# Kernel optimization log

Measured on AMD Instinct MI355X. Metric: run time of the kernel, lower is better.

## Reference

```python
import jax, jax.numpy as jnp
import numpy as np

V, E, DIN, DH = 8192, 4096, 512, 256
N_CLASSES = 2
EPS = 1e-5  # torch LayerNorm default
EDGE_P = 0.004  # ~33 nodes per hyperedge


def layernorm(x, g, b):
    m = jnp.mean(x, axis=-1, keepdims=True)
    v = jnp.mean((x - m) ** 2, axis=-1, keepdims=True)
    return (x - m) / jnp.sqrt(v + EPS) * g + b


def setup_inputs() -> dict:
    key = jax.random.key(0)
    ks = jax.random.split(key, 8)
    X = jax.random.normal(ks[0], (V, DIN), dtype=jnp.float32)
    # binary incidence matrix (|V|, |E|)
    H_inc = (jax.random.uniform(ks[1], (V, E)) < EDGE_P).astype(jnp.float32)
    Wp = jax.random.normal(ks[2], (DH, DIN), dtype=jnp.float32) * 0.02  # input_proj (no bias)
    W0 = jax.random.normal(ks[3], (DH, DH), dtype=jnp.float32) * 0.02
    W1 = jax.random.normal(ks[4], (DH, DH), dtype=jnp.float32) * 0.02
    g0 = jnp.ones((DH,), jnp.float32); b0 = jnp.zeros((DH,), jnp.float32)
    g1 = jnp.ones((DH,), jnp.float32); b1 = jnp.zeros((DH,), jnp.float32)
    Wc = jax.random.normal(ks[5], (N_CLASSES, DH), dtype=jnp.float32) * 0.02
    bc = jnp.zeros((N_CLASSES,), jnp.float32)
    return {"X": X, "H_inc": H_inc, "Wp": Wp, "W0": W0, "W1": W1,
            "g0": g0, "b0": b0, "g1": g1, "b1": b1, "Wc": Wc, "bc": bc}


def reference(X, H_inc, Wp, W0, W1, g0, b0, g1, b1, Wc, bc):
    # --- normalized incidence: H_tilde = D_v^{-1/2} H D_e^{-1/2}, 0 for isolated ---
    d_v = H_inc.sum(axis=1)   # (V,)
    d_e = H_inc.sum(axis=0)   # (E,)
    dvi = jnp.where(d_v > 0, jnp.where(d_v > 0, d_v, 1.0) ** -0.5, 0.0)
    dei = jnp.where(d_e > 0, jnp.where(d_e > 0, d_e, 1.0) ** -0.5, 0.0)
    H_tilde = dvi[:, None] * H_inc * dei[None, :]            # (V, E)
    HHt = H_tilde @ H_tilde.T                                # (V, V)

    # input projection
    Xh = X @ Wp.T                                            # (V, DH)

    # L=2 message-passing layers with residual + LayerNorm
    for W, g, b in ((W0, g0, b0), (W1, g1, b1)):
        Xn = jax.nn.relu((HHt @ Xh) @ W.T)
        Xh = layernorm(Xh + Xn, g, b)

    # mean pool per hyperedge (== Python loop over E in the original):
    # z_e = mean of member node embeddings; zeros for empty hyperedges
    cnt = jnp.where(d_e > 0, d_e, 1.0)[:, None]              # (E, 1)
    z_E = (H_inc.T @ Xh) / cnt                               # (E, DH)

    logits = z_E @ Wc.T + bc                                 # (E, 2)
    return jax.nn.softmax(logits, axis=1)
```

## Files before the change

kernel.cpp:

```cpp
#include <hip/hip_runtime.h>
#include <math.h>

#define NV 8192
#define NE 4096
#define DIN 512
#define DH 256
#define CAP_E 96
#define CAP_V 64

#define OFF_XH   0
#define OFF_Z    (OFF_XH + NV*DH)
#define OFF_Y    (OFF_Z  + NV*DH)
#define OFF_NCNT (OFF_Y  + NE*DH)
#define OFF_ECNT (OFF_NCNT + NV)
#define OFF_EL   (OFF_ECNT + NE)
#define OFF_NL   (OFF_EL + NE*CAP_E)

using bf16x8 = __attribute__((ext_vector_type(8))) short;
using f32x4  = __attribute__((ext_vector_type(4))) float;

__device__ inline unsigned short f2bf(float f) {
    union { float f; unsigned u; } v; v.f = f;
    unsigned r = v.u + 0x7FFF + ((v.u >> 16) & 1);
    return (unsigned short)(r >> 16);
}

__global__ __launch_bounds__(256) void scan_H(const float* __restrict__ H,
                                              int* __restrict__ edge_cnt,
                                              int* __restrict__ node_cnt,
                                              int* __restrict__ edge_list,
                                              int* __restrict__ node_list) {
    int idx = blockIdx.x * 256 + threadIdx.x;
    int f0 = idx * 16;
    int v = f0 >> 12;
    int e = f0 & (NE - 1);
    float4 h0 = *(const float4*)(H + (size_t)f0);
    float4 h1 = *(const float4*)(H + (size_t)f0 + 4);
    float4 h2 = *(const float4*)(H + (size_t)f0 + 8);
    float4 h3 = *(const float4*)(H + (size_t)f0 + 12);
    float hv[16] = {h0.x, h0.y, h0.z, h0.w, h1.x, h1.y, h1.z, h1.w,
                    h2.x, h2.y, h2.z, h2.w, h3.x, h3.y, h3.z, h3.w};
    bool any = false;
#pragma unroll
    for (int j = 0; j < 16; ++j) any |= (hv[j] != 0.0f);
    if (__ballot(any) == 0ull) return;
#pragma unroll
    for (int j = 0; j < 16; ++j) {
        if (hv[j] != 0.0f) {
            int ee = e + j;
            int s1 = atomicAdd(&edge_cnt[ee], 1);
            if (s1 < CAP_E) edge_list[ee * CAP_E + s1] = v;
            int s2 = atomicAdd(&node_cnt[v], 1);
            if (s2 < CAP_V) node_list[v * CAP_V + s2] = ee;
        }
    }
}

__global__ __launch_bounds__(256) void gemm_bf16(const float* __restrict__ A,
                                                 const float* __restrict__ B,
                                                 float* __restrict__ C,
                                                 int K) {
    __shared__ short As[2048];
    __shared__ short Bs[16384];
    const int tid  = threadIdx.x;
    const int lane = tid & 63;
    const int w    = tid >> 6;
    const int bm   = blockIdx.x * 32;
    const int swz  = lane ^ ((lane >> 3) & 6);

    float4 ar[2], br[16];
    {
        int i0 = tid, i1 = tid + 256;
        ar[0] = *(const float4*)(A + (size_t)(bm + (i0 >> 4)) * K + ((i0 & 15) << 2));
        ar[1] = *(const float4*)(A + (size_t)(bm + (i1 >> 4)) * K + ((i1 & 15) << 2));
#pragma unroll
        for (int it = 0; it < 16; ++it) {
            int i = tid + it * 256;
            br[it] = *(const float4*)(B + (size_t)(i >> 4) * K + ((i & 15) << 2));
        }
    }
    f32x4 acc[2][4];
#pragma unroll
    for (int mi = 0; mi < 2; ++mi)
#pragma unroll
        for (int ni = 0; ni < 4; ++ni) acc[mi][ni] = (f32x4){0.f, 0.f, 0.f, 0.f};

    for (int k0 = 0; k0 < K; k0 += 64) {
        __syncthreads();
#pragma unroll
        for (int s = 0; s < 2; ++s) {
            int i = tid + s * 256;
            int row = i >> 4, kk = (i & 15) << 2;
            int kc = kk >> 5, quad = (kk >> 3) & 3, j = kk & 7;
            int ln = (row & 15) + (quad << 4);
            int p  = ln ^ ((ln >> 3) & 6);
            int addr = ((row >> 4) * 2 + kc) * 512 + p * 8 + j;
            float4 v = ar[s];
            ushort4 u = {f2bf(v.x), f2bf(v.y), f2bf(v.z), f2bf(v.w)};
            *(ushort4*)&As[addr] = u;
        }
#pragma unroll
        for (int it = 0; it < 16; ++it) {
            int i = tid + it * 256;
            int row = i >> 4, kk = (i & 15) << 2;
            int kc = kk >> 5, quad = (kk >> 3) & 3, j = kk & 7;
            int ln = (row & 15) + (quad << 4);
            int p  = ln ^ ((ln >> 3) & 6);
            int addr = ((row >> 4) * 2 + kc) * 512 + p * 8 + j;
            float4 v = br[it];
            ushort4 u = {f2bf(v.x), f2bf(v.y), f2bf(v.z), f2bf(v.w)};
            *(ushort4*)&Bs[addr] = u;
        }
        __syncthreads();
        if (k0 + 64 < K) {
            int kn = k0 + 64;
            int i0 = tid, i1 = tid + 256;
            ar[0] = *(const float4*)(A + (size_t)(bm + (i0 >> 4)) * K + kn + ((i0 & 15) << 2));
            ar[1] = *(const float4*)(A + (size_t)(bm + (i1 >> 4)) * K + kn + ((i1 & 15) << 2));
#pragma unroll
            for (int it = 0; it < 16; ++it) {
                int i = tid + it * 256;
                br[it] = *(const float4*)(B + (size_t)(i >> 4) * K + kn + ((i & 15) << 2));
            }
        }
#pragma unroll
        for (int kc = 0; kc < 2; ++kc) {
            bf16x8 af[2], bfr[4];
            af[0] = *(const bf16x8*)&As[(0 * 2 + kc) * 512 + swz * 8];
            af[1] = *(const bf16x8*)&As[(1 * 2 + kc) * 512 + swz * 8];
#pragma unroll
            for (int ni = 0; ni < 4; ++ni)
                bfr[ni] = *(const bf16x8*)&Bs[((w * 4 + ni) * 2 + kc) * 512 + swz * 8];
#pragma unroll
            for (int mi = 0; mi < 2; ++mi)
#pragma unroll
                for (int ni = 0; ni < 4; ++ni)
                    acc[mi][ni] = __builtin_amdgcn_mfma_f32_16x16x32_bf16(
                        af[mi], bfr[ni], acc[mi][ni], 0, 0, 0);
        }
    }
    const int quad = lane >> 4, cl = lane & 15;
#pragma unroll
    for (int mi = 0; mi < 2; ++mi)
#pragma unroll
        for (int ni = 0; ni < 4; ++ni)
#pragma unroll
            for (int r = 0; r < 4; ++r)
                C[(size_t)(bm + mi * 16 + quad * 4 + r) * DH + w * 64 + ni * 16 + cl]
                    = acc[mi][ni][r];
}

__global__ __launch_bounds__(256) void gemm_relu_res_ln(const float* __restrict__ Z,
                                                        const float* __restrict__ W,
                                                        float* __restrict__ Xh,
                                                        const float* __restrict__ g,
                                                        const float* __restrict__ b) {
    const int K = DH;
    __shared__ short As[2048];
    __shared__ short Bs[16384];
    __shared__ float redS[32][4];
    __shared__ float redQ[32][4];
    const int tid  = threadIdx.x;
    const int lane = tid & 63;
    const int w    = tid >> 6;
    const int bm   = blockIdx.x * 32;
    const int swz  = lane ^ ((lane >> 3) & 6);

    float4 ar[2], br[16];
    {
        int i0 = tid, i1 = tid + 256;
        ar[0] = *(const float4*)(Z + (size_t)(bm + (i0 >> 4)) * K + ((i0 & 15) << 2));
        ar[1] = *(const float4*)(Z + (size_t)(bm + (i1 >> 4)) * K + ((i1 & 15) << 2));
#pragma unroll
        for (int it = 0; it < 16; ++it) {
            int i = tid + it * 256;
            br[it] = *(const float4*)(W + (size_t)(i >> 4) * K + ((i & 15) << 2));
        }
    }
    f32x4 acc[2][4];
#pragma unroll
    for (int mi = 0; mi < 2; ++mi)
#pragma unroll
        for (int ni = 0; ni < 4; ++ni) acc[mi][ni] = (f32x4){0.f, 0.f, 0.f, 0.f};

    for (int k0 = 0; k0 < K; k0 += 64) {
        __syncthreads();
#pragma unroll
        for (int s = 0; s < 2; ++s) {
            int i = tid + s * 256;
            int row = i >> 4, kk = (i & 15) << 2;
            int kc = kk >> 5, quad = (kk >> 3) & 3, j = kk & 7;
            int ln = (row & 15) + (quad << 4);
            int p  = ln ^ ((ln >> 3) & 6);
            int addr = ((row >> 4) * 2 + kc) * 512 + p * 8 + j;
            float4 v = ar[s];
            ushort4 u = {f2bf(v.x), f2bf(v.y), f2bf(v.z), f2bf(v.w)};
            *(ushort4*)&As[addr] = u;
        }
#pragma unroll
        for (int it = 0; it < 16; ++it) {
            int i = tid + it * 256;
            int row = i >> 4, kk = (i & 15) << 2;
            int kc = kk >> 5, quad = (kk >> 3) & 3, j = kk & 7;
            int ln = (row & 15) + (quad << 4);
            int p  = ln ^ ((ln >> 3) & 6);
            int addr = ((row >> 4) * 2 + kc) * 512 + p * 8 + j;
            float4 v = br[it];
            ushort4 u = {f2bf(v.x), f2bf(v.y), f2bf(v.z), f2bf(v.w)};
            *(ushort4*)&Bs[addr] = u;
        }
        __syncthreads();
        if (k0 + 64 < K) {
            int kn = k0 + 64;
            int i0 = tid, i1 = tid + 256;
            ar[0] = *(const float4*)(Z + (size_t)(bm + (i0 >> 4)) * K + kn + ((i0 & 15) << 2));
            ar[1] = *(const float4*)(Z + (size_t)(bm + (i1 >> 4)) * K + kn + ((i1 & 15) << 2));
#pragma unroll
            for (int it = 0; it < 16; ++it) {
                int i = tid + it * 256;
                br[it] = *(const float4*)(W + (size_t)(i >> 4) * K + kn + ((i & 15) << 2));
            }
        }
#pragma unroll
        for (int kc = 0; kc < 2; ++kc) {
            bf16x8 af[2], bfr[4];
            af[0] = *(const bf16x8*)&As[(0 * 2 + kc) * 512 + swz * 8];
            af[1] = *(const bf16x8*)&As[(1 * 2 + kc) * 512 + swz * 8];
#pragma unroll
            for (int ni = 0; ni < 4; ++ni)
                bfr[ni] = *(const bf16x8*)&Bs[((w * 4 + ni) * 2 + kc) * 512 + swz * 8];
#pragma unroll
            for (int mi = 0; mi < 2; ++mi)
#pragma unroll
                for (int ni = 0; ni < 4; ++ni)
                    acc[mi][ni] = __builtin_amdgcn_mfma_f32_16x16x32_bf16(
                        af[mi], bfr[ni], acc[mi][ni], 0, 0, 0);
        }
    }
    const int quad = lane >> 4, cl = lane & 15;
#pragma unroll
    for (int mi = 0; mi < 2; ++mi)
#pragma unroll
        for (int r = 0; r < 4; ++r) {
            int row = bm + mi * 16 + quad * 4 + r;
            float s = 0.f, q = 0.f;
#pragma unroll
            for (int ni = 0; ni < 4; ++ni) {
                int col = w * 64 + ni * 16 + cl;
                float v = fmaxf(acc[mi][ni][r], 0.f) + Xh[(size_t)row * DH + col];
                acc[mi][ni][r] = v;
                s += v; q = fmaf(v, v, q);
            }
#pragma unroll
            for (int o = 1; o < 16; o <<= 1) {
                s += __shfl_xor(s, o, 64);
                q += __shfl_xor(q, o, 64);
            }
            if (cl == 0) {
                redS[mi * 16 + quad * 4 + r][w] = s;
                redQ[mi * 16 + quad * 4 + r][w] = q;
            }
        }
    __syncthreads();
#pragma unroll
    for (int mi = 0; mi < 2; ++mi)
#pragma unroll
        for (int r = 0; r < 4; ++r) {
            int R = mi * 16 + quad * 4 + r;
            float s = redS[R][0] + redS[R][1] + redS[R][2] + redS[R][3];
            float q = redQ[R][0] + redQ[R][1] + redQ[R][2] + redQ[R][3];
            float m = s * (1.0f / DH);
            float var = q * (1.0f / DH) - m * m;
            float rstd = rsqrtf(var + 1e-5f);
            int row = bm + R;
#pragma unroll
            for (int ni = 0; ni < 4; ++ni) {
                int col = w * 64 + ni * 16 + cl;
                float v = (acc[mi][ni][r] - m) * rstd * g[col] + b[col];
                Xh[(size_t)row * DH + col] = v;
            }
        }
}

__global__ __launch_bounds__(64) void edge_gather(const float* __restrict__ Xh,
                                                  const int* __restrict__ edge_cnt,
                                                  const int* __restrict__ edge_list,
                                                  const int* __restrict__ node_cnt,
                                                  float* __restrict__ Y) {
    int e = blockIdx.x;
    int tid = threadIdx.x;
    __shared__ int   lv[CAP_E];
    __shared__ float lc[CAP_E];
    int cnt = min(edge_cnt[e], CAP_E);
    for (int j = tid; j < cnt; j += 64) {
        int v = edge_list[e * CAP_E + j];
        lv[j] = v * (DH / 4);
        lc[j] = rsqrtf((float)node_cnt[v]);
    }
    __syncthreads();
    const float4* X4 = (const float4*)Xh;
    float4 a0 = {0,0,0,0}, a1 = {0,0,0,0}, a2 = {0,0,0,0}, a3 = {0,0,0,0};
    int i = 0;
    for (; i + 4 <= cnt; i += 4) {
        float4 x0 = X4[lv[i+0] + tid], x1 = X4[lv[i+1] + tid];
        float4 x2 = X4[lv[i+2] + tid], x3 = X4[lv[i+3] + tid];
        float c0 = lc[i+0], c1 = lc[i+1], c2 = lc[i+2], c3 = lc[i+3];
        a0.x = fmaf(c0, x0.x, a0.x); a0.y = fmaf(c0, x0.y, a0.y);
        a0.z = fmaf(c0, x0.z, a0.z); a0.w = fmaf(c0, x0.w, a0.w);
        a1.x = fmaf(c1, x1.x, a1.x); a1.y = fmaf(c1, x1.y, a1.y);
        a1.z = fmaf(c1, x1.z, a1.z); a1.w = fmaf(c1, x1.w, a1.w);
        a2.x = fmaf(c2, x2.x, a2.x); a2.y = fmaf(c2, x2.y, a2.y);
        a2.z = fmaf(c2, x2.z, a2.z); a2.w = fmaf(c2, x2.w, a2.w);
        a3.x = fmaf(c3, x3.x, a3.x); a3.y = fmaf(c3, x3.y, a3.y);
        a3.z = fmaf(c3, x3.z, a3.z); a3.w = fmaf(c3, x3.w, a3.w);
    }
    for (; i < cnt; ++i) {
        float4 x0 = X4[lv[i] + tid]; float c0 = lc[i];
        a0.x = fmaf(c0, x0.x, a0.x); a0.y = fmaf(c0, x0.y, a0.y);
        a0.z = fmaf(c0, x0.z, a0.z); a0.w = fmaf(c0, x0.w, a0.w);
    }
    float de = cnt > 0 ? rsqrtf((float)cnt) : 0.f;
    float4 o;
    o.x = de * ((a0.x + a1.x) + (a2.x + a3.x));
    o.y = de * ((a0.y + a1.y) + (a2.y + a3.y));
    o.z = de * ((a0.z + a1.z) + (a2.z + a3.z));
    o.w = de * ((a0.w + a1.w) + (a2.w + a3.w));
    ((float4*)Y)[e * (DH / 4) + tid] = o;
}

__global__ __launch_bounds__(64) void node_gather(const float* __restrict__ Y,
                                                  const int* __restrict__ node_cnt,
                                                  const int* __restrict__ node_list,
                                                  const int* __restrict__ edge_cnt,
                                                  float* __restrict__ Z) {
    int v = blockIdx.x;
    int tid = threadIdx.x;
    __shared__ int   le[CAP_V];
    __shared__ float lc[CAP_V];
    int cnt = min(node_cnt[v], CAP_V);
    if (tid < cnt) {
        int e = node_list[v * CAP_V + tid];
        le[tid] = e * (DH / 4);
        lc[tid] = rsqrtf((float)edge_cnt[e]);
    }
    __syncthreads();
    const float4* Y4 = (const float4*)Y;
    float4 a0 = {0,0,0,0}, a1 = {0,0,0,0}, a2 = {0,0,0,0}, a3 = {0,0,0,0};
    int i = 0;
    for (; i + 4 <= cnt; i += 4) {
        float4 x0 = Y4[le[i+0] + tid], x1 = Y4[le[i+1] + tid];
        float4 x2 = Y4[le[i+2] + tid], x3 = Y4[le[i+3] + tid];
        float c0 = lc[i+0], c1 = lc[i+1], c2 = lc[i+2], c3 = lc[i+3];
        a0.x = fmaf(c0, x0.x, a0.x); a0.y = fmaf(c0, x0.y, a0.y);
        a0.z = fmaf(c0, x0.z, a0.z); a0.w = fmaf(c0, x0.w, a0.w);
        a1.x = fmaf(c1, x1.x, a1.x); a1.y = fmaf(c1, x1.y, a1.y);
        a1.z = fmaf(c1, x1.z, a1.z); a1.w = fmaf(c1, x1.w, a1.w);
        a2.x = fmaf(c2, x2.x, a2.x); a2.y = fmaf(c2, x2.y, a2.y);
        a2.z = fmaf(c2, x2.z, a2.z); a2.w = fmaf(c2, x2.w, a2.w);
        a3.x = fmaf(c3, x3.x, a3.x); a3.y = fmaf(c3, x3.y, a3.y);
        a3.z = fmaf(c3, x3.z, a3.z); a3.w = fmaf(c3, x3.w, a3.w);
    }
    for (; i < cnt; ++i) {
        float4 x0 = Y4[le[i] + tid]; float c0 = lc[i];
        a0.x = fmaf(c0, x0.x, a0.x); a0.y = fmaf(c0, x0.y, a0.y);
        a0.z = fmaf(c0, x0.z, a0.z); a0.w = fmaf(c0, x0.w, a0.w);
    }
    float dv = cnt > 0 ? rsqrtf((float)cnt) : 0.f;
    float4 o;
    o.x = dv * ((a0.x + a1.x) + (a2.x + a3.x));
    o.y = dv * ((a0.y + a1.y) + (a2.y + a3.y));
    o.z = dv * ((a0.z + a1.z) + (a2.z + a3.z));
    o.w = dv * ((a0.w + a1.w) + (a2.w + a3.w));
    ((float4*)Z)[v * (DH / 4) + tid] = o;
}

__global__ __launch_bounds__(64) void pool_classify(const float* __restrict__ Xh,
                                                    const int* __restrict__ edge_cnt,
                                                    const int* __restrict__ edge_list,
                                                    const float* __restrict__ Wc,
                                                    const float* __restrict__ bc,
                                                    float* __restrict__ out) {
    int e = blockIdx.x;
    int tid = threadIdx.x;
    __shared__ int lv[CAP_E];
    int cnt = min(edge_cnt[e], CAP_E);
    for (int j = tid; j < cnt; j += 64) lv[j] = edge_list[e * CAP_E + j] * (DH / 4);
    __syncthreads();
    const float4* X4 = (const float4*)Xh;
    float4 a0 = {0,0,0,0}, a1 = {0,0,0,0}, a2 = {0,0,0,0}, a3 = {0,0,0,0};
    int i = 0;
    for (; i + 4 <= cnt; i += 4) {
        float4 x0 = X4[lv[i+0] + tid], x1 = X4[lv[i+1] + tid];
        float4 x2 = X4[lv[i+2] + tid], x3 = X4[lv[i+3] + tid];
        a0.x += x0.x; a0.y += x0.y; a0.z += x0.z; a0.w += x0.w;
        a1.x += x1.x; a1.y += x1.y; a1.z += x1.z; a1.w += x1.w;
        a2.x += x2.x; a2.y += x2.y; a2.z += x2.z; a2.w += x2.w;
        a3.x += x3.x; a3.y += x3.y; a3.z += x3.z; a3.w += x3.w;
    }
    for (; i < cnt; ++i) {
        float4 x0 = X4[lv[i] + tid];
        a0.x += x0.x; a0.y += x0.y; a0.z += x0.z; a0.w += x0.w;
    }
    float inv = cnt > 0 ? 1.0f / (float)cnt : 1.0f;
    float4 val;
    val.x = inv * ((a0.x + a1.x) + (a2.x + a3.x));
    val.y = inv * ((a0.y + a1.y) + (a2.y + a3.y));
    val.z = inv * ((a0.z + a1.z) + (a2.z + a3.z));
    val.w = inv * ((a0.w + a1.w) + (a2.w + a3.w));
    const float4* W4 = (const float4*)Wc;
    float4 w0 = W4[tid], w1 = W4[64 + tid];
    float p0 = val.x * w0.x + val.y * w0.y + val.z * w0.z + val.w * w0.w;
    float p1 = val.x * w1.x + val.y * w1.y + val.z * w1.z + val.w * w1.w;
#pragma unroll
    for (int o = 32; o > 0; o >>= 1) {
        p0 += __shfl_down(p0, o, 64);
        p1 += __shfl_down(p1, o, 64);
    }
    if (tid == 0) {
        float l0 = p0 + bc[0], l1 = p1 + bc[1];
        float mx = fmaxf(l0, l1);
        float e0 = expf(l0 - mx), e1 = expf(l1 - mx);
        float s = 1.0f / (e0 + e1);
        out[e * 2 + 0] = e0 * s;
        out[e * 2 + 1] = e1 * s;
    }
}

extern "C" void kernel_launch(void* const* d_in, const int* in_sizes, int n_in,
                              void* d_out, int out_size, void* d_ws, size_t ws_size,
                              hipStream_t stream) {
    const float* X  = (const float*)d_in[0];
    const float* H  = (const float*)d_in[1];
    const float* Wp = (const float*)d_in[2];
    const float* W0 = (const float*)d_in[3];
    const float* W1 = (const float*)d_in[4];
    const float* g0 = (const float*)d_in[5];
    const float* b0 = (const float*)d_in[6];
    const float* g1 = (const float*)d_in[7];
    const float* b1 = (const float*)d_in[8];
    const float* Wc = (const float*)d_in[9];
    const float* bc = (const float*)d_in[10];
    float* out = (float*)d_out;

    float* ws = (float*)d_ws;
    float* Xh  = ws + OFF_XH;
    float* Z   = ws + OFF_Z;
    float* Y   = ws + OFF_Y;
    int* node_cnt  = (int*)(ws + OFF_NCNT);
    int* edge_cnt  = (int*)(ws + OFF_ECNT);
    int* edge_list = (int*)(ws + OFF_EL);
    int* node_list = (int*)(ws + OFF_NL);

    hipMemsetAsync(node_cnt, 0, (size_t)(NV + NE) * sizeof(int), stream);

    scan_H<<<(NV * NE) / 4096, 256, 0, stream>>>(H, edge_cnt, node_cnt, edge_list, node_list);

    gemm_bf16<<<NV / 32, 256, 0, stream>>>(X, Wp, Xh, DIN);

    const float* Ws[2] = {W0, W1};
    const float* gs[2] = {g0, g1};
    const float* bs[2] = {b0, b1};
    for (int l = 0; l < 2; ++l) {
        edge_gather<<<NE, 64, 0, stream>>>(Xh, edge_cnt, edge_list, node_cnt, Y);
        node_gather<<<NV, 64, 0, stream>>>(Y, node_cnt, node_list, edge_cnt, Z);
        gemm_relu_res_ln<<<NV / 32, 256, 0, stream>>>(Z, Ws[l], Xh, gs[l], bs[l]);
    }

    pool_classify<<<NE, 64, 0, stream>>>(Xh, edge_cnt, edge_list, Wc, bc, out);
}
```

Baseline: 329.7 us.

## Build node lists in shared memory, pad edge counters, unroll gathers by eight

The incidence scan now uses one block per node row. Each node's edge list is collected in shared memory with a local atomic and written out once, which removes the global atomics on node counters. Edge counters are padded to one per 64 bytes to reduce atomic contention and false sharing between neighbouring hyperedges. The gather kernels use eight independent accumulators instead of four, putting more loads in flight. This adds more registers and a larger memset.

```diff
diff --git a/kernel.cpp b/kernel.cpp
--- a/kernel.cpp
+++ b/kernel.cpp
@@ -13,7 +13,7 @@
 #define OFF_Y    (OFF_Z  + NV*DH)
 #define OFF_NCNT (OFF_Y  + NE*DH)
 #define OFF_ECNT (OFF_NCNT + NV)
-#define OFF_EL   (OFF_ECNT + NE)
+#define OFF_EL   (OFF_ECNT + NE*16)
 #define OFF_NL   (OFF_EL + NE*CAP_E)
 
 using bf16x8 = __attribute__((ext_vector_type(8))) short;
@@ -30,30 +30,36 @@
                                               int* __restrict__ node_cnt,
                                               int* __restrict__ edge_list,
                                               int* __restrict__ node_list) {
-    int idx = blockIdx.x * 256 + threadIdx.x;
-    int f0 = idx * 16;
-    int v = f0 >> 12;
-    int e = f0 & (NE - 1);
-    float4 h0 = *(const float4*)(H + (size_t)f0);
-    float4 h1 = *(const float4*)(H + (size_t)f0 + 4);
-    float4 h2 = *(const float4*)(H + (size_t)f0 + 8);
-    float4 h3 = *(const float4*)(H + (size_t)f0 + 12);
+    int v = blockIdx.x;
+    int t = threadIdx.x;
+    __shared__ int lcnt;
+    __shared__ int lbuf[CAP_V];
+    if (t == 0) lcnt = 0;
+    __syncthreads();
+    const float4* H4 = (const float4*)(H + (size_t)v * NE);
+    float4 h0 = H4[t * 4 + 0], h1 = H4[t * 4 + 1];
+    float4 h2 = H4[t * 4 + 2], h3 = H4[t * 4 + 3];
     float hv[16] = {h0.x, h0.y, h0.z, h0.w, h1.x, h1.y, h1.z, h1.w,
                     h2.x, h2.y, h2.z, h2.w, h3.x, h3.y, h3.z, h3.w};
-    bool any = false;
-#pragma unroll
-    for (int j = 0; j < 16; ++j) any |= (hv[j] != 0.0f);
-    if (__ballot(any) == 0ull) return;
-#pragma unroll
-    for (int j = 0; j < 16; ++j) {
-        if (hv[j] != 0.0f) {
-            int ee = e + j;
-            int s1 = atomicAdd(&edge_cnt[ee], 1);
-            if (s1 < CAP_E) edge_list[ee * CAP_E + s1] = v;
-            int s2 = atomicAdd(&node_cnt[v], 1);
-            if (s2 < CAP_V) node_list[v * CAP_V + s2] = ee;
-        }
-    }
+    int myE[16]; int n = 0;
+    int e0 = t * 16;
+#pragma unroll
+    for (int j = 0; j < 16; ++j)
+        if (hv[j] != 0.0f) myE[n++] = e0 + j;
+    if (n > 0) {
+        int s = atomicAdd(&lcnt, n);
+        for (int k = 0; k < n; ++k) {
+            int ee = myE[k];
+            if (s + k < CAP_V) lbuf[s + k] = ee;
+            int g = atomicAdd(&edge_cnt[ee << 4], 1);
+            if (g < CAP_E) edge_list[ee * CAP_E + g] = v;
+        }
+    }
+    __syncthreads();
+    int c = lcnt;
+    if (t == 0) node_cnt[v] = c;
+    c = min(c, CAP_V);
+    for (int i = t; i < c; i += 256) node_list[v * CAP_V + i] = lbuf[i];
 }
 
 __global__ __launch_bounds__(256) void gemm_bf16(const float* __restrict__ A,
@@ -282,6 +288,28 @@
         }
 }
 
+#define GATHER_BODY(SRC, IDX, COEF, CNT)                                         \
+    float4 a[8];                                                                 \
+    _Pragma("unroll") for (int u = 0; u < 8; ++u) a[u] = (float4){0,0,0,0};      \
+    int i = 0;                                                                   \
+    for (; i + 8 <= CNT; i += 8) {                                               \
+        _Pragma("unroll") for (int u = 0; u < 8; ++u) {                          \
+            float4 x = SRC[IDX[i+u] + tid]; float c = COEF[i+u];                 \
+            a[u].x = fmaf(c, x.x, a[u].x); a[u].y = fmaf(c, x.y, a[u].y);        \
+            a[u].z = fmaf(c, x.z, a[u].z); a[u].w = fmaf(c, x.w, a[u].w);        \
+        }                                                                        \
+    }                                                                            \
+    for (; i < CNT; ++i) {                                                       \
+        float4 x = SRC[IDX[i] + tid]; float c = COEF[i];                         \
+        a[0].x = fmaf(c, x.x, a[0].x); a[0].y = fmaf(c, x.y, a[0].y);            \
+        a[0].z = fmaf(c, x.z, a[0].z); a[0].w = fmaf(c, x.w, a[0].w);            \
+    }                                                                            \
+    _Pragma("unroll") for (int u = 4; u > 0; u >>= 1)                            \
+        _Pragma("unroll") for (int q = 0; q < u; ++q) {                          \
+            a[q].x += a[q+u].x; a[q].y += a[q+u].y;                              \
+            a[q].z += a[q+u].z; a[q].w += a[q+u].w;                              \
+        }
+
 __global__ __launch_bounds__(64) void edge_gather(const float* __restrict__ Xh,
                                                   const int* __restrict__ edge_cnt,
                                                   const int* __restrict__ edge_list,
@@ -291,7 +319,7 @@
     int tid = threadIdx.x;
     __shared__ int   lv[CAP_E];
     __shared__ float lc[CAP_E];
-    int cnt = min(edge_cnt[e], CAP_E);
+    int cnt = min(edge_cnt[e << 4], CAP_E);
     for (int j = tid; j < cnt; j += 64) {
         int v = edge_list[e * CAP_E + j];
         lv[j] = v * (DH / 4);
@@ -299,32 +327,9 @@
     }
     __syncthreads();
     const float4* X4 = (const float4*)Xh;
-    float4 a0 = {0,0,0,0}, a1 = {0,0,0,0}, a2 = {0,0,0,0}, a3 = {0,0,0,0};
-    int i = 0;
-    for (; i + 4 <= cnt; i += 4) {
-        float4 x0 = X4[lv[i+0] + tid], x1 = X4[lv[i+1] + tid];
-        float4 x2 = X4[lv[i+2] + tid], x3 = X4[lv[i+3] + tid];
-        float c0 = lc[i+0], c1 = lc[i+1], c2 = lc[i+2], c3 = lc[i+3];
-        a0.x = fmaf(c0, x0.x, a0.x); a0.y = fmaf(c0, x0.y, a0.y);
-        a0.z = fmaf(c0, x0.z, a0.z); a0.w = fmaf(c0, x0.w, a0.w);
-        a1.x = fmaf(c1, x1.x, a1.x); a1.y = fmaf(c1, x1.y, a1.y);
-        a1.z = fmaf(c1, x1.z, a1.z); a1.w = fmaf(c1, x1.w, a1.w);
-        a2.x = fmaf(c2, x2.x, a2.x); a2.y = fmaf(c2, x2.y, a2.y);
-        a2.z = fmaf(c2, x2.z, a2.z); a2.w = fmaf(c2, x2.w, a2.w);
-        a3.x = fmaf(c3, x3.x, a3.x); a3.y = fmaf(c3, x3.y, a3.y);
-        a3.z = fmaf(c3, x3.z, a3.z); a3.w = fmaf(c3, x3.w, a3.w);
-    }
-    for (; i < cnt; ++i) {
-        float4 x0 = X4[lv[i] + tid]; float c0 = lc[i];
-        a0.x = fmaf(c0, x0.x, a0.x); a0.y = fmaf(c0, x0.y, a0.y);
-        a0.z = fmaf(c0, x0.z, a0.z); a0.w = fmaf(c0, x0.w, a0.w);
-    }
+    GATHER_BODY(X4, lv, lc, cnt)
     float de = cnt > 0 ? rsqrtf((float)cnt) : 0.f;
-    float4 o;
-    o.x = de * ((a0.x + a1.x) + (a2.x + a3.x));
-    o.y = de * ((a0.y + a1.y) + (a2.y + a3.y));
-    o.z = de * ((a0.z + a1.z) + (a2.z + a3.z));
-    o.w = de * ((a0.w + a1.w) + (a2.w + a3.w));
+    float4 o = {de * a[0].x, de * a[0].y, de * a[0].z, de * a[0].w};
     ((float4*)Y)[e * (DH / 4) + tid] = o;
 }
 
@@ -341,36 +346,13 @@
     if (tid < cnt) {
         int e = node_list[v * CAP_V + tid];
         le[tid] = e * (DH / 4);
-        lc[tid] = rsqrtf((float)edge_cnt[e]);
+        lc[tid] = rsqrtf((float)edge_cnt[e << 4]);
     }
     __syncthreads();
     const float4* Y4 = (const float4*)Y;
-    float4 a0 = {0,0,0,0}, a1 = {0,0,0,0}, a2 = {0,0,0,0}, a3 = {0,0,0,0};
-    int i = 0;
-    for (; i + 4 <= cnt; i += 4) {
-        float4 x0 = Y4[le[i+0] + tid], x1 = Y4[le[i+1] + tid];
-        float4 x2 = Y4[le[i+2] + tid], x3 = Y4[le[i+3] + tid];
-        float c0 = lc[i+0], c1 = lc[i+1], c2 = lc[i+2], c3 = lc[i+3];
-        a0.x = fmaf(c0, x0.x, a0.x); a0.y = fmaf(c0, x0.y, a0.y);
-        a0.z = fmaf(c0, x0.z, a0.z); a0.w = fmaf(c0, x0.w, a0.w);
-        a1.x = fmaf(c1, x1.x, a1.x); a1.y = fmaf(c1, x1.y, a1.y);
-        a1.z = fmaf(c1, x1.z, a1.z); a1.w = fmaf(c1, x1.w, a1.w);
-        a2.x = fmaf(c2, x2.x, a2.x); a2.y = fmaf(c2, x2.y, a2.y);
-        a2.z = fmaf(c2, x2.z, a2.z); a2.w = fmaf(c2, x2.w, a2.w);
-        a3.x = fmaf(c3, x3.x, a3.x); a3.y = fmaf(c3, x3.y, a3.y);
-        a3.z = fmaf(c3, x3.z, a3.z); a3.w = fmaf(c3, x3.w, a3.w);
-    }
-    for (; i < cnt; ++i) {
-        float4 x0 = Y4[le[i] + tid]; float c0 = lc[i];
-        a0.x = fmaf(c0, x0.x, a0.x); a0.y = fmaf(c0, x0.y, a0.y);
-        a0.z = fmaf(c0, x0.z, a0.z); a0.w = fmaf(c0, x0.w, a0.w);
-    }
+    GATHER_BODY(Y4, le, lc, cnt)
     float dv = cnt > 0 ? rsqrtf((float)cnt) : 0.f;
-    float4 o;
-    o.x = dv * ((a0.x + a1.x) + (a2.x + a3.x));
-    o.y = dv * ((a0.y + a1.y) + (a2.y + a3.y));
-    o.z = dv * ((a0.z + a1.z) + (a2.z + a3.z));
-    o.w = dv * ((a0.w + a1.w) + (a2.w + a3.w));
+    float4 o = {dv * a[0].x, dv * a[0].y, dv * a[0].z, dv * a[0].w};
     ((float4*)Z)[v * (DH / 4) + tid] = o;
 }
 
@@ -383,30 +365,34 @@
     int e = blockIdx.x;
     int tid = threadIdx.x;
     __shared__ int lv[CAP_E];
-    int cnt = min(edge_cnt[e], CAP_E);
+    int cnt = min(edge_cnt[e << 4], CAP_E);
     for (int j = tid; j < cnt; j += 64) lv[j] = edge_list[e * CAP_E + j] * (DH / 4);
     __syncthreads();
     const float4* X4 = (const float4*)Xh;
-    float4 a0 = {0,0,0,0}, a1 = {0,0,0,0}, a2 = {0,0,0,0}, a3 = {0,0,0,0};
+    float4 a[8];
+#pragma unroll
+    for (int u = 0; u < 8; ++u) a[u] = (float4){0, 0, 0, 0};
     int i = 0;
-    for (; i + 4 <= cnt; i += 4) {
-        float4 x0 = X4[lv[i+0] + tid], x1 = X4[lv[i+1] + tid];
-        float4 x2 = X4[lv[i+2] + tid], x3 = X4[lv[i+3] + tid];
-        a0.x += x0.x; a0.y += x0.y; a0.z += x0.z; a0.w += x0.w;
-        a1.x += x1.x; a1.y += x1.y; a1.z += x1.z; a1.w += x1.w;
-        a2.x += x2.x; a2.y += x2.y; a2.z += x2.z; a2.w += x2.w;
-        a3.x += x3.x; a3.y += x3.y; a3.z += x3.z; a3.w += x3.w;
+    for (; i + 8 <= cnt; i += 8) {
+#pragma unroll
+        for (int u = 0; u < 8; ++u) {
+            float4 x = X4[lv[i + u] + tid];
+            a[u].x += x.x; a[u].y += x.y; a[u].z += x.z; a[u].w += x.w;
+        }
     }
     for (; i < cnt; ++i) {
-        float4 x0 = X4[lv[i] + tid];
-        a0.x += x0.x; a0.y += x0.y; a0.z += x0.z; a0.w += x0.w;
-    }
+        float4 x = X4[lv[i] + tid];
+        a[0].x += x.x; a[0].y += x.y; a[0].z += x.z; a[0].w += x.w;
+    }
+#pragma unroll
+    for (int u = 4; u > 0; u >>= 1)
+#pragma unroll
+        for (int q = 0; q < u; ++q) {
+            a[q].x += a[q + u].x; a[q].y += a[q + u].y;
+            a[q].z += a[q + u].z; a[q].w += a[q + u].w;
+        }
     float inv = cnt > 0 ? 1.0f / (float)cnt : 1.0f;
-    float4 val;
-    val.x = inv * ((a0.x + a1.x) + (a2.x + a3.x));
-    val.y = inv * ((a0.y + a1.y) + (a2.y + a3.y));
-    val.z = inv * ((a0.z + a1.z) + (a2.z + a3.z));
-    val.w = inv * ((a0.w + a1.w) + (a2.w + a3.w));
+    float4 val = {a[0].x * inv, a[0].y * inv, a[0].z * inv, a[0].w * inv};
     const float4* W4 = (const float4*)Wc;
     float4 w0 = W4[tid], w1 = W4[64 + tid];
     float p0 = val.x * w0.x + val.y * w0.y + val.z * w0.z + val.w * w0.w;
@@ -451,9 +437,9 @@
     int* edge_list = (int*)(ws + OFF_EL);
     int* node_list = (int*)(ws + OFF_NL);
 
-    hipMemsetAsync(node_cnt, 0, (size_t)(NV + NE) * sizeof(int), stream);
-
-    scan_H<<<(NV * NE) / 4096, 256, 0, stream>>>(H, edge_cnt, node_cnt, edge_list, node_list);
+    hipMemsetAsync(edge_cnt, 0, (size_t)(NE * 16) * sizeof(int), stream);
+
+    scan_H<<<NV, 256, 0, stream>>>(H, edge_cnt, node_cnt, edge_list, node_list);
 
     gemm_bf16<<<NV / 32, 256, 0, stream>>>(X, Wp, Xh, DIN);
 
```

Result: no change. 327.8 us (-0.6%).
